# Kernel optimization log

Measured on AMD Instinct MI355X. Metric: run time of the kernel, lower is better.

Reference implementation:

```python
import jax, jax.numpy as jnp
import numpy as np


def _grid_sample_bilinear(img, gx, gy):
    """Bilinear sampling at pixel coords (gx, gy), align_corners=True convention,
    zero padding for out-of-bounds (matches old-default torch grid_sample).
    img: [B,C,H,W]; gx, gy: [B,H,W] in pixel units."""
    B, C, H, W = img.shape
    x0 = jnp.floor(gx)
    y0 = jnp.floor(gy)
    x1 = x0 + 1.0
    y1 = y0 + 1.0
    wx1 = gx - x0
    wx0 = 1.0 - wx1
    wy1 = gy - y0
    wy0 = 1.0 - wy1
    img_flat = img.reshape(B, C, H * W)

    def corner(xc, yc, w):
        valid = ((xc >= 0) & (xc <= W - 1) & (yc >= 0) & (yc <= H - 1)).astype(img.dtype)
        xi = jnp.clip(xc, 0, W - 1).astype(jnp.int32)
        yi = jnp.clip(yc, 0, H - 1).astype(jnp.int32)
        idx = (yi * W + xi).reshape(B, 1, H * W)  # broadcast over C
        vals = jnp.take_along_axis(img_flat, idx, axis=2).reshape(B, C, H, W)
        return vals * (w * valid)[:, None, :, :]

    return (corner(x0, y0, wx0 * wy0) + corner(x1, y0, wx1 * wy0)
            + corner(x0, y1, wx0 * wy1) + corner(x1, y1, wx1 * wy1))


def _warp(image, flo):
    B, C, H, W = image.shape
    # base grid in pixel coords; torch normalizes 2*v/(W-1)-1 then grid_sample
    # (align_corners=True) de-normalizes back to pixel coords -> they cancel.
    xx = jnp.arange(W, dtype=image.dtype)[None, None, :]   # [1,1,W]
    yy = jnp.arange(H, dtype=image.dtype)[None, :, None]   # [1,H,1]
    gx = xx + flo[:, 0]  # [B,H,W]
    gy = yy + flo[:, 1]
    out = _grid_sample_bilinear(image, gx, gy)
    # mask = grid_sample(ones) then hard threshold; values are channel-independent
    ones = jnp.ones((B, 1, H, W), dtype=image.dtype)
    mask = _grid_sample_bilinear(ones, gx, gy)
    mask = jnp.where(mask < 0.9999, jnp.zeros((), image.dtype), jnp.ones((), image.dtype))
    return out * mask


def setup_inputs() -> dict:
    key = jax.random.key(0)
    k1, k2 = jax.random.split(key)
    B, C, H, W = 8, 16, 512, 512
    image = jax.random.normal(k1, (B, C, H, W), dtype=jnp.float32)
    # realistic flow magnitudes of a few pixels
    UVgrid = jax.random.normal(k2, (B, 2, H, W), dtype=jnp.float32) * 8.0
    return {"image": image, "UVgrid": UVgrid}


def reference(image, UVgrid):
    # scale=1, upsampleMode='nearest': Upsample to [H*1, W*1] is identity,
    # UVgrid * scale is identity.
    return _warp(image, UVgrid)
```

## Files before the change

kernel.cpp:

```cpp
#include <hip/hip_runtime.h>

#define BATCH 8
#define CH    16
#define HH    512
#define WW    512
#define HW    (HH * WW)

#define TILE  32
#define RPAD  16
#define REGE  64
#define NPX   4
#define CG    2
#define NG    (CH / CG)


typedef __attribute__((address_space(1))) const void global_cvoid;
typedef __attribute__((address_space(3))) void lds_void;

__device__ __forceinline__ void gll16(const float* g, float* l) {
    __builtin_amdgcn_global_load_lds((global_cvoid*)g, (lds_void*)l, 16, 0, 0);
}

#define STAGE(g, nb) do {                                               \
    _Pragma("unroll")                                                   \
    for (int c_ = 0; c_ < CG; ++c_) {                                   \
        const float* pc_ = img + ib + (size_t)((g) * CG + c_) * HW;     \
        _Pragma("unroll")                                               \
        for (int k_ = 0; k_ < 4; ++k_) {                                \
            const int q_  = k_ * 4 + wv;           \
            const int ry_ = q_ * 4 + sub;           \
            const int gy_ = min(max(y0r + ry_, 0), HH - 1);             \
            const int off_ = min(max(gy_ * WW + xch, 0), HW - 4);       \
            gll16(pc_ + off_, &buf[nb][c_][q_ * 4][0]);                 \
        }                                                               \
    }                                                                   \
} while (0)

#define GATHER(g, cb) do {                                              \
    _Pragma("unroll")                                                   \
    for (int c_ = 0; c_ < CG; ++c_) {                                   \
        const float* pl_ = &buf[cb][c_][0][0];                          \
        float* o0_ = out + ib + (size_t)((g) * CG + c_) * HW;           \
        _Pragma("unroll")                                               \
        for (int p_ = 0; p_ < NPX; ++p_) {                              \
            const int l_   = lidx[p_];                                  \
            const int dx_  = dxv[p_];                                   \
            const int dyo_ = dyov[p_];                                  \
            const float v00 = pl_[l_];                                  \
            const float v01 = pl_[l_ + dx_];                            \
            const float v10 = pl_[l_ + dyo_];                           \
            const float v11 = pl_[l_ + dx_ + dyo_];                     \
            o0_[obase[p_]] = w00[p_]*v00 + w01[p_]*v01                  \
                           + w10[p_]*v10 + w11[p_]*v11;                 \
        }                                                               \
    }                                                                   \
} while (0)

__global__ __launch_bounds__(256) void warp_gll(
    const float* __restrict__ img,
    const float* __restrict__ flo,
    float* __restrict__ out)
{
    __shared__ float buf[2][CG][REGE][REGE];

    const int t   = threadIdx.x;
    const int bid = blockIdx.x;
    const int tile = (bid & 7) * 256 + (bid >> 3);
    const int b    = tile >> 8;
    const int ty   = (tile >> 4) & 15;
    const int tx   = tile & 15;
    const int xb   = tx * TILE;
    const int yb   = ty * TILE;
    const int x0r  = xb - RPAD;
    const int y0r  = yb - RPAD;

    const int lane = t & 63;
    const int wv   = t >> 6;
    const int sub  = lane >> 4;
    const int xch  = x0r + (lane & 15) * 4;
    const size_t ib = (size_t)b * CH * HW;

    STAGE(0, 0);
    STAGE(1, 1);

    float w00[NPX], w01[NPX], w10[NPX], w11[NPX];
    int   lidx[NPX], dxv[NPX], dyov[NPX], obase[NPX];
    int   fbmask = 0;

    const float* fbp = flo + (size_t)b * 2 * HW;

#pragma unroll
    for (int p = 0; p < NPX; ++p) {
        const int pix = p * 256 + t;
        const int row = pix >> 5;
        const int col = pix & 31;
        const int h   = yb + row;
        const int w   = xb + col;
        const int hw  = h * WW + w;
        obase[p] = hw;

        const float fx = fbp[hw];
        const float fy = fbp[HW + hw];
        const float gx = (float)w + fx;
        const float gy = (float)h + fy;

        const float x0f = floorf(gx), y0f = floorf(gy);
        const float wx1 = gx - x0f, wx0 = 1.0f - wx1;
        const float wy1 = gy - y0f, wy0 = 1.0f - wy1;

        const bool vx0 = (x0f >= 0.0f)        && (x0f <= (float)(WW - 1));
        const bool vx1 = (x0f + 1.0f >= 0.0f) && (x0f + 1.0f <= (float)(WW - 1));
        const bool vy0 = (y0f >= 0.0f)        && (y0f <= (float)(HH - 1));
        const bool vy1 = (y0f + 1.0f >= 0.0f) && (y0f + 1.0f <= (float)(HH - 1));

        float a00 = wx0 * wy0 * ((vx0 && vy0) ? 1.0f : 0.0f);
        float a01 = wx1 * wy0 * ((vx1 && vy0) ? 1.0f : 0.0f);
        float a10 = wx0 * wy1 * ((vx0 && vy1) ? 1.0f : 0.0f);
        float a11 = wx1 * wy1 * ((vx1 && vy1) ? 1.0f : 0.0f);

        const float msum = a00 + a01 + a10 + a11;
        const float mask = (msum < 0.9999f) ? 0.0f : 1.0f;
        w00[p] = a00 * mask; w01[p] = a01 * mask;
        w10[p] = a10 * mask; w11[p] = a11 * mask;

        const int x0 = min(max((int)x0f, 0), WW - 1);
        const int x1 = min(max((int)x0f + 1, 0), WW - 1);
        const int y0 = min(max((int)y0f, 0), HH - 1);
        const int y1 = min(max((int)y0f + 1, 0), HH - 1);

        const int dx = x1 - x0;
        const int dy = y1 - y0;
        dxv[p]  = dx;
        dyov[p] = dy * REGE;

        const int xl = x0 - x0r;
        const int yl = y0 - y0r;
        if (!((xl >= 0) && (xl + dx <= REGE - 1) &&
              (yl >= 0) && (yl + dy <= REGE - 1)))
            fbmask |= (1 << p);
        lidx[p] = min(max(yl, 0), REGE - 2) * REGE + min(max(xl, 0), REGE - 2);
    }

    __syncthreads();

    GATHER(0, 0);
    __syncthreads();
    STAGE(2, 0);  GATHER(1, 1);  __syncthreads();
    STAGE(3, 1);  GATHER(2, 0);  __syncthreads();
    STAGE(4, 0);  GATHER(3, 1);  __syncthreads();
    STAGE(5, 1);  GATHER(4, 0);  __syncthreads();
    STAGE(6, 0);  GATHER(5, 1);  __syncthreads();
    STAGE(7, 1);  GATHER(6, 0);  __syncthreads();
    GATHER(7, 1);

    if (fbmask) {
#pragma unroll
        for (int p = 0; p < NPX; ++p) {
            if (!(fbmask & (1 << p))) continue;
            const int pix = p * 256 + t;
            const int row = pix >> 5;
            const int col = pix & 31;
            const int h   = yb + row;
            const int w   = xb + col;
            const int hw  = h * WW + w;

            const float fx = fbp[hw];
            const float fy = fbp[HW + hw];
            const float gx = (float)w + fx;
            const float gy = (float)h + fy;

            const float x0f = floorf(gx), y0f = floorf(gy);
            const float wx1 = gx - x0f, wx0 = 1.0f - wx1;
            const float wy1 = gy - y0f, wy0 = 1.0f - wy1;

            const bool vx0 = (x0f >= 0.0f)        && (x0f <= (float)(WW - 1));
            const bool vx1 = (x0f + 1.0f >= 0.0f) && (x0f + 1.0f <= (float)(WW - 1));
            const bool vy0 = (y0f >= 0.0f)        && (y0f <= (float)(HH - 1));
            const bool vy1 = (y0f + 1.0f >= 0.0f) && (y0f + 1.0f <= (float)(HH - 1));

            float a00 = wx0 * wy0 * ((vx0 && vy0) ? 1.0f : 0.0f);
            float a01 = wx1 * wy0 * ((vx1 && vy0) ? 1.0f : 0.0f);
            float a10 = wx0 * wy1 * ((vx0 && vy1) ? 1.0f : 0.0f);
            float a11 = wx1 * wy1 * ((vx1 && vy1) ? 1.0f : 0.0f);

            const float msum = a00 + a01 + a10 + a11;
            const float mask = (msum < 0.9999f) ? 0.0f : 1.0f;
            a00 *= mask; a01 *= mask; a10 *= mask; a11 *= mask;

            const int x0 = min(max((int)x0f, 0), WW - 1);
            const int x1 = min(max((int)x0f + 1, 0), WW - 1);
            const int y0 = min(max((int)y0f, 0), HH - 1);
            const int y1 = min(max((int)y0f + 1, 0), HH - 1);

            const int gA  = y0 * WW + x0;
            const int dx  = x1 - x0;
            const int dyo = (y1 - y0) * WW;

            const float* ic = img + ib;
            float*       oc = out + ib + hw;
            for (int c = 0; c < CH; ++c) {
                const float* pc = ic + (size_t)c * HW;
                const float v = a00 * pc[gA]
                              + a01 * pc[gA + dx]
                              + a10 * pc[gA + dyo]
                              + a11 * pc[gA + dx + dyo];
                oc[(size_t)c * HW] = v;
            }
        }
    }
}

extern "C" void kernel_launch(void* const* d_in, const int* in_sizes, int n_in,
                              void* d_out, int out_size, void* d_ws, size_t ws_size,
                              hipStream_t stream) {
    const float* img = (const float*)d_in[0];
    const float* flo = (const float*)d_in[1];
    float* out = (float*)d_out;

    const int blocks = BATCH * (HH / TILE) * (WW / TILE);
    warp_gll<<<blocks, 256, 0, stream>>>(img, flo, out);
}
```

Before: 302.5 us.

## Triple-buffer per-channel LDS staging with vmcnt waits and deferred stores

Replaces the double-buffered two-channel staging with a three-slot ring of single-channel 64x64 LDS tiles. Each phase waits with an explicit s_waitcnt vmcnt instead of a full __syncthreads, so later global_load_lds requests stay in flight across the barrier. Flow values and global offsets are loaded once up front and reused by the fallback path. All 16x4 results are held in registers and written at the end, with launch bounds set for 3 blocks per CU. This is meant to cut barrier stalls and raise memory-level parallelism, at the cost of many more registers (64 result floats) and fragile hand-counted vmcnt values.

```diff
diff --git a/kernel.cpp b/kernel.cpp
--- a/kernel.cpp
+++ b/kernel.cpp
@@ -10,8 +10,6 @@
 #define RPAD  16
 #define REGE  64
 #define NPX   4
-#define CG    2
-#define NG    (CH / CG)
 
 
 typedef __attribute__((address_space(1))) const void global_cvoid;
@@ -21,47 +19,46 @@
     __builtin_amdgcn_global_load_lds((global_cvoid*)g, (lds_void*)l, 16, 0, 0);
 }
 
+#define WAITVM(n) asm volatile("s_waitcnt vmcnt(" #n ")" ::: "memory")
+#define BAR()     __builtin_amdgcn_s_barrier()
+
 #define STAGE(g, nb) do {                                               \
+    const float* pc_ = img + ib + (size_t)(g) * HW;                     \
     _Pragma("unroll")                                                   \
-    for (int c_ = 0; c_ < CG; ++c_) {                                   \
-        const float* pc_ = img + ib + (size_t)((g) * CG + c_) * HW;     \
-        _Pragma("unroll")                                               \
-        for (int k_ = 0; k_ < 4; ++k_) {                                \
-            const int q_  = k_ * 4 + wv;           \
-            const int ry_ = q_ * 4 + sub;           \
-            const int gy_ = min(max(y0r + ry_, 0), HH - 1);             \
-            const int off_ = min(max(gy_ * WW + xch, 0), HW - 4);       \
-            gll16(pc_ + off_, &buf[nb][c_][q_ * 4][0]);                 \
-        }                                                               \
+    for (int k_ = 0; k_ < 4; ++k_) {                                    \
+        gll16(pc_ + goff[k_], &buf[nb][(k_ * 4 + wv) * 4][0]);          \
     }                                                                   \
 } while (0)
 
 #define GATHER(g, cb) do {                                              \
+    const float* pl_ = &buf[cb][0][0];                                  \
     _Pragma("unroll")                                                   \
-    for (int c_ = 0; c_ < CG; ++c_) {                                   \
-        const float* pl_ = &buf[cb][c_][0][0];                          \
-        float* o0_ = out + ib + (size_t)((g) * CG + c_) * HW;           \
-        _Pragma("unroll")                                               \
-        for (int p_ = 0; p_ < NPX; ++p_) {                              \
-            const int l_   = lidx[p_];                                  \
-            const int dx_  = dxv[p_];                                   \
-            const int dyo_ = dyov[p_];                                  \
-            const float v00 = pl_[l_];                                  \
-            const float v01 = pl_[l_ + dx_];                            \
-            const float v10 = pl_[l_ + dyo_];                           \
-            const float v11 = pl_[l_ + dx_ + dyo_];                     \
-            o0_[obase[p_]] = w00[p_]*v00 + w01[p_]*v01                  \
-                           + w10[p_]*v10 + w11[p_]*v11;                 \
-        }                                                               \
+    for (int p_ = 0; p_ < NPX; ++p_) {                                  \
+        const int l_   = lidx[p_];                                      \
+        const int dx_  = dxv[p_];                                       \
+        const int dyo_ = dyov[p_];                                      \
+        const float v00 = pl_[l_];                                      \
+        const float v01 = pl_[l_ + dx_];                                \
+        const float v10 = pl_[l_ + dyo_];                               \
+        const float v11 = pl_[l_ + dx_ + dyo_];                         \
+        res[g][p_] = w00[p_]*v00 + w01[p_]*v01                          \
+                   + w10[p_]*v10 + w11[p_]*v11;                         \
     }                                                                   \
 } while (0)
 
-__global__ __launch_bounds__(256) void warp_gll(
+#define PHASE(g) do {                                                   \
+    GATHER(g, (g) % 3);                                                 \
+    WAITVM(4);                                                          \
+    BAR();                                                              \
+    STAGE((g) + 3, (g) % 3);                                            \
+} while (0)
+
+__global__ __launch_bounds__(256, 3) void warp_cnt(
     const float* __restrict__ img,
     const float* __restrict__ flo,
     float* __restrict__ out)
 {
-    __shared__ float buf[2][CG][REGE][REGE];
+    __shared__ float buf[3][REGE][REGE];
 
     const int t   = threadIdx.x;
     const int bid = blockIdx.x;
@@ -80,14 +77,33 @@
     const int xch  = x0r + (lane & 15) * 4;
     const size_t ib = (size_t)b * CH * HW;
 
+    int goff[4];
+#pragma unroll
+    for (int k = 0; k < 4; ++k) {
+        const int q  = k * 4 + wv;
+        const int ry = q * 4 + sub;
+        const int gy = min(max(y0r + ry, 0), HH - 1);
+        goff[k] = min(max(gy * WW + xch, 0), HW - 4);
+    }
+
+    const float* fbp = flo + (size_t)b * 2 * HW;
+    float fxv[NPX], fyv[NPX];
+#pragma unroll
+    for (int p = 0; p < NPX; ++p) {
+        const int pix = p * 256 + t;
+        const int hw  = (yb + (pix >> 5)) * WW + xb + (pix & 31);
+        fxv[p] = fbp[hw];
+        fyv[p] = fbp[HW + hw];
+    }
+    asm volatile("" ::: "memory");
+
     STAGE(0, 0);
     STAGE(1, 1);
+    STAGE(2, 2);
 
     float w00[NPX], w01[NPX], w10[NPX], w11[NPX];
     int   lidx[NPX], dxv[NPX], dyov[NPX], obase[NPX];
     int   fbmask = 0;
-
-    const float* fbp = flo + (size_t)b * 2 * HW;
 
 #pragma unroll
     for (int p = 0; p < NPX; ++p) {
@@ -96,13 +112,10 @@
         const int col = pix & 31;
         const int h   = yb + row;
         const int w   = xb + col;
-        const int hw  = h * WW + w;
-        obase[p] = hw;
-
-        const float fx = fbp[hw];
-        const float fy = fbp[HW + hw];
-        const float gx = (float)w + fx;
-        const float gy = (float)h + fy;
+        obase[p] = h * WW + w;
+
+        const float gx = (float)w + fxv[p];
+        const float gy = (float)h + fyv[p];
 
         const float x0f = floorf(gx), y0f = floorf(gy);
         const float wx1 = gx - x0f, wx0 = 1.0f - wx1;
@@ -141,17 +154,26 @@
         lidx[p] = min(max(yl, 0), REGE - 2) * REGE + min(max(xl, 0), REGE - 2);
     }
 
-    __syncthreads();
-
-    GATHER(0, 0);
-    __syncthreads();
-    STAGE(2, 0);  GATHER(1, 1);  __syncthreads();
-    STAGE(3, 1);  GATHER(2, 0);  __syncthreads();
-    STAGE(4, 0);  GATHER(3, 1);  __syncthreads();
-    STAGE(5, 1);  GATHER(4, 0);  __syncthreads();
-    STAGE(6, 0);  GATHER(5, 1);  __syncthreads();
-    STAGE(7, 1);  GATHER(6, 0);  __syncthreads();
-    GATHER(7, 1);
+    float res[CH][NPX];
+
+    WAITVM(8);
+    BAR();
+
+    PHASE(0);   PHASE(1);   PHASE(2);   PHASE(3);
+    PHASE(4);   PHASE(5);   PHASE(6);   PHASE(7);
+    PHASE(8);   PHASE(9);   PHASE(10);  PHASE(11);
+    PHASE(12);
+    GATHER(13, 1);  WAITVM(4);  BAR();
+    GATHER(14, 2);  WAITVM(0);  BAR();
+    GATHER(15, 0);
+
+#pragma unroll
+    for (int c = 0; c < CH; ++c) {
+        float* o0 = out + ib + (size_t)c * HW;
+#pragma unroll
+        for (int p = 0; p < NPX; ++p)
+            o0[obase[p]] = res[c][p];
+    }
 
     if (fbmask) {
 #pragma unroll
@@ -164,10 +186,8 @@
             const int w   = xb + col;
             const int hw  = h * WW + w;
 
-            const float fx = fbp[hw];
-            const float fy = fbp[HW + hw];
-            const float gx = (float)w + fx;
-            const float gy = (float)h + fy;
+            const float gx = (float)w + fxv[p];
+            const float gy = (float)h + fyv[p];
 
             const float x0f = floorf(gx), y0f = floorf(gy);
             const float wx1 = gx - x0f, wx0 = 1.0f - wx1;
@@ -218,5 +238,5 @@
     float* out = (float*)d_out;
 
     const int blocks = BATCH * (HH / TILE) * (WW / TILE);
-    warp_gll<<<blocks, 256, 0, stream>>>(img, flo, out);
+    warp_cnt<<<blocks, 256, 0, stream>>>(img, flo, out);
 }
```

After: 280.3 us. 1.08x faster.
